# Kernel optimization log

Hardware: AMD Instinct MI355X
Metric: run time of the kernel (lower is better)

## Reference

```python
import math
import jax, jax.numpy as jnp
import numpy as np

B, T, C, H = 2, 2048, 1024, 16
MAX_SEQ = 2048


def _make_pe(max_seq: int, dim: int, base: float = 10000.0) -> np.ndarray:
    pe = np.zeros((max_seq, dim), dtype=np.float32)
    position = np.arange(max_seq, dtype=np.float32)[:, None]
    div_term = np.exp(np.arange(0, dim, 2, dtype=np.float32) * (-math.log(base) / dim))
    pe[:, 0::2] = np.sin(position * div_term)
    pe[:, 1::2] = np.cos(position * div_term)
    return pe


def setup_inputs() -> dict:
    key = jax.random.key(0)
    k1, k2, k3 = jax.random.split(key, 3)
    x = jax.random.normal(k1, (B, T, C), dtype=jnp.float32)
    # torch Linear default init scale ~ 1/sqrt(fan_in)
    w_qkv = jax.random.normal(k2, (3 * C, C), dtype=jnp.float32) / math.sqrt(C)
    w_proj = jax.random.normal(k3, (C, C), dtype=jnp.float32) / math.sqrt(C)
    pe = jnp.asarray(_make_pe(MAX_SEQ, C))
    return {"x": x, "w_qkv": w_qkv, "w_proj": w_proj, "pe": pe}


def reference(x, w_qkv, w_proj, pe):
    b, t, c = x.shape
    h = H
    d = c // h
    # RoPE module adds sinusoidal PE under torch.no_grad() -> stop_gradient
    xp = jax.lax.stop_gradient(x + pe[None, :t, :])
    qkv = xp @ w_qkv.T  # [b, t, 3c]
    q, k, v = jnp.split(qkv, 3, axis=-1)
    q = q.reshape(b, t, h, d).transpose(0, 2, 1, 3)  # bhtd
    k = k.reshape(b, t, h, d).transpose(0, 2, 1, 3)
    v = v.reshape(b, t, h, d).transpose(0, 2, 1, 3)
    att = jnp.einsum("bhqd,bhkd->bhqk", q, k) * (1.0 / math.sqrt(d))
    causal = jnp.tril(jnp.ones((t, t), dtype=bool))  # [t, t]
    att = jnp.where(causal[None, None], att, -jnp.inf)
    att = jax.nn.softmax(att, axis=-1)
    y = jnp.einsum("bhqk,bhkd->bhqd", att, v)
    y = y.transpose(0, 2, 1, 3).reshape(b, t, c)
    return y @ w_proj.T
```

## Files before the change

### kernel.cpp

```cpp
#include <hip/hip_runtime.h>
#include <cstdint>

typedef __bf16 bf16x8 __attribute__((ext_vector_type(8)));
typedef __bf16 bf16x4 __attribute__((ext_vector_type(4)));
typedef float  f32x4  __attribute__((ext_vector_type(4)));

static constexpr int kB = 2, kT = 2048, kC = 1024, kH = 16, kD = 64;
static constexpr int kK = 1024;

__device__ __forceinline__ uint16_t f2bf(float f) {
  uint32_t u = __builtin_bit_cast(uint32_t, f);
  u += 0x7FFFu + ((u >> 16) & 1u);
  return (uint16_t)(u >> 16);
}

__device__ __forceinline__ void gl_lds16(const void* g, void* l) {
  __builtin_amdgcn_global_load_lds((__attribute__((address_space(1))) void*)(void*)g,
                                   (__attribute__((address_space(3))) void*)l, 16, 0, 0);
}

__global__ __launch_bounds__(256) void prep_xpe(const float* __restrict__ x,
                                                const float* __restrict__ pe,
                                                uint16_t* __restrict__ xp) {
  const int i = blockIdx.x * 256 + threadIdx.x;
  const float4 xv = ((const float4*)x)[i];
  const int c4 = i & (kC / 4 - 1);
  const int t = (i / (kC / 4)) & (kT - 1);
  const float4 pv = ((const float4*)pe)[t * (kC / 4) + c4];
  ushort4 o;
  o.x = f2bf(xv.x + pv.x);
  o.y = f2bf(xv.y + pv.y);
  o.z = f2bf(xv.z + pv.z);
  o.w = f2bf(xv.w + pv.w);
  ((ushort4*)xp)[i] = o;
}

__global__ __launch_bounds__(256) void cast_w(const float* __restrict__ w,
                                              uint16_t* __restrict__ o) {
  const int i = blockIdx.x * 256 + threadIdx.x;
  const float4 v = ((const float4*)w)[i];
  ushort4 u;
  u.x = f2bf(v.x); u.y = f2bf(v.y); u.z = f2bf(v.z); u.w = f2bf(v.w);
  ((ushort4*)o)[i] = u;
}

template <int EPI>
__global__ __launch_bounds__(256) void gemm_bt(const uint16_t* __restrict__ A,
                                               const uint16_t* __restrict__ W,
                                               uint16_t* __restrict__ qb,
                                               uint16_t* __restrict__ kb,
                                               uint16_t* __restrict__ vT,
                                               float* __restrict__ out) {
  __shared__ __align__(1024) char lds[EPI == 0 ? 34816 : 32768];
  const int lane = threadIdx.x & 63;
  const int wid = threadIdx.x >> 6;
  const int l15 = lane & 15, l4 = lane >> 4;
  const int wm = wid >> 1, wn = wid & 1;
  const int orig = (int)(blockIdx.y * gridDim.x + blockIdx.x);
  const int xcd = orig & 7, j = orig >> 3;
  const int m0 = (xcd * 4 + (j & 3)) * 128;
  const int n0 = (j >> 2) * 128;

  f32x4 acc[4][4] = {};

  for (int k0 = 0; k0 < kK; k0 += 64) {
#pragma unroll
    for (int jj = 0; jj < 4; ++jj) {
      const int off = wid * 4096 + jj * 1024 + lane * 16;
      const int row = off >> 7;
      const int colb = (off & 127) ^ ((row & 7) << 4);
      gl_lds16((const char*)A + ((size_t)(m0 + row) * kK + k0) * 2 + colb,
               lds + wid * 4096 + jj * 1024);
      gl_lds16((const char*)W + ((size_t)(n0 + row) * kK + k0) * 2 + colb,
               lds + 16384 + wid * 4096 + jj * 1024);
    }
    __syncthreads();
#pragma unroll
    for (int ks = 0; ks < 2; ++ks) {
      bf16x8 af[4], bf_[4];
#pragma unroll
      for (int mt = 0; mt < 4; ++mt) {
        const int r = wm * 64 + mt * 16 + l15;
        const int cb = (l4 * 16 + ks * 64) ^ ((r & 7) << 4);
        af[mt] = *(const bf16x8*)(lds + r * 128 + cb);
      }
#pragma unroll
      for (int nt = 0; nt < 4; ++nt) {
        const int r = wn * 64 + nt * 16 + l15;
        const int cb = (l4 * 16 + ks * 64) ^ ((r & 7) << 4);
        bf_[nt] = *(const bf16x8*)(lds + 16384 + r * 128 + cb);
      }
#pragma unroll
      for (int mt = 0; mt < 4; ++mt)
#pragma unroll
        for (int nt = 0; nt < 4; ++nt)
          acc[mt][nt] = __builtin_amdgcn_mfma_f32_16x16x32_bf16(af[mt], bf_[nt],
                                                                acc[mt][nt], 0, 0, 0);
    }
    __syncthreads();
  }

  if constexpr (EPI == 0) {
    const int sec = n0 >> 10;
    if (sec < 2) {
#pragma unroll
      for (int mt = 0; mt < 4; ++mt)
#pragma unroll
        for (int nt = 0; nt < 4; ++nt)
#pragma unroll
          for (int r = 0; r < 4; ++r) {
            const int m = wm * 64 + mt * 16 + l4 * 4 + r;
            const int n = wn * 64 + nt * 16 + l15;
            *(uint16_t*)(lds + m * 272 + ((n * 2) ^ (((m >> 2) & 3) << 4))) =
                f2bf(acc[mt][nt][r]);
          }
    } else {
#pragma unroll
      for (int mt = 0; mt < 4; ++mt)
#pragma unroll
        for (int nt = 0; nt < 4; ++nt)
#pragma unroll
          for (int r = 0; r < 4; ++r) {
            const int m = wm * 64 + mt * 16 + l4 * 4 + r;
            const int n = wn * 64 + nt * 16 + l15;
            *(uint16_t*)(lds + n * 272 + m * 2) = f2bf(acc[mt][nt][r]);
          }
    }
    __syncthreads();
    const int tid = threadIdx.x;
    const int b = m0 >> 11, tbase = m0 & (kT - 1);
    if (sec < 2) {
      uint16_t* dst = (sec == 0) ? qb : kb;
#pragma unroll
      for (int i = 0; i < 8; ++i) {
        const int g = i * 256 + tid;
        const int ml = g >> 4;
        const int c8 = (g & 15) * 8;
        const bf16x8 v =
            *(const bf16x8*)(lds + ml * 272 + ((c8 * 2) ^ (((ml >> 2) & 3) << 4)));
        const int nn = (n0 & (kC - 1)) + c8;
        const int h = nn >> 6, d = nn & 63;
        *(bf16x8*)(dst + ((size_t)((b * kH + h) * kT + tbase + ml)) * kD + d) = v;
      }
    } else {
#pragma unroll
      for (int i = 0; i < 8; ++i) {
        const int g = i * 256 + tid;
        const int dl = g >> 4;
        const int m8 = (g & 15) * 8;
        const bf16x8 v = *(const bf16x8*)(lds + dl * 272 + m8 * 2);
        const int nn = (n0 & (kC - 1)) + dl;
        const int h = nn >> 6, d = nn & 63;
        *(bf16x8*)(vT + ((size_t)((b * kH + h) * kD + d)) * kT + tbase + m8) = v;
      }
    }
  } else {
#pragma unroll
    for (int mt = 0; mt < 4; ++mt)
#pragma unroll
      for (int nt = 0; nt < 4; ++nt)
#pragma unroll
        for (int r = 0; r < 4; ++r) {
          const int m = m0 + wm * 64 + mt * 16 + l4 * 4 + r;
          const int n = n0 + wn * 64 + nt * 16 + l15;
          out[(size_t)m * kC + n] = acc[mt][nt][r];
        }
  }
}

__global__ __launch_bounds__(256, 4) void attn(const uint16_t* __restrict__ qb,
                                               const uint16_t* __restrict__ kb,
                                               const uint16_t* __restrict__ vT,
                                               uint16_t* __restrict__ y) {
  __shared__ __align__(1024) char lds[40960];
  const int lane = threadIdx.x & 63;
  const int wid = threadIdx.x >> 6;
  const int l15 = lane & 15, l4 = lane >> 4;
  const int bh = blockIdx.x;
  const int qt = (int)(gridDim.y - 1) - (int)blockIdx.y;
  const int q0 = qt * 64 + wid * 16;
  const size_t base = (size_t)bh * kT * kD;
  const uint16_t* Q = qb + base;
  const uint16_t* Kp = kb + base;
  const uint16_t* Vt = vT + base;
  char* P = lds + 32768 + wid * 2048;
  const int xr = (l15 & 7) << 4;

  bf16x8 qf[2];
#pragma unroll
  for (int ks = 0; ks < 2; ++ks) {
    bf16x8 t = *(const bf16x8*)(Q + (size_t)(q0 + l15) * kD + ks * 32 + l4 * 8);
#pragma unroll
    for (int i = 0; i < 8; ++i) t[i] = (__bf16)((float)t[i] * 0.1803368801f);
    qf[ks] = t;
  }

  float m_ = -1e30f, l_ = 0.f;
  f32x4 o[4];
#pragma unroll
  for (int nt = 0; nt < 4; ++nt) o[nt] = (f32x4){0.f, 0.f, 0.f, 0.f};

  const int nkt = qt + 1;

  auto STAGE = [&](int bi, int k0) {
#pragma unroll
    for (int c = 0; c < 2; ++c) {
      const int call = wid * 2 + c;
      const int row = call * 8 + (lane >> 3);
      const int colb = (((lane & 7) ^ ((lane >> 3) & 7)) << 4);
      gl_lds16((const char*)Kp + ((size_t)(k0 + row) * kD) * 2 + colb,
               lds + bi * 8192 + call * 1024);
      gl_lds16((const char*)Vt + ((size_t)row * kT + k0) * 2 + colb,
               lds + 16384 + bi * 8192 + call * 1024);
    }
  };

  int cur = 0;
  STAGE(0, 0);
  for (int kt = 0; kt < nkt; ++kt) {
    const int k0 = kt * 64;
    const bool hasnext = (kt + 1 < nkt);
    if (hasnext) STAGE(cur ^ 1, k0 + 64);
    if (hasnext)
      asm volatile("s_waitcnt vmcnt(4)" ::: "memory");
    else
      asm volatile("s_waitcnt vmcnt(0)" ::: "memory");
    __builtin_amdgcn_s_barrier();
    asm volatile("" ::: "memory");

    const char* Kb = lds + cur * 8192;
    const char* Vb = lds + 16384 + cur * 8192;

    f32x4 s[4] = {};
    __builtin_amdgcn_s_setprio(1);
#pragma unroll
    for (int ks = 0; ks < 2; ++ks)
#pragma unroll
      for (int nt = 0; nt < 4; ++nt) {
        const bf16x8 kf =
            *(const bf16x8*)(Kb + (nt * 16 + l15) * 128 + ((ks * 64 + l4 * 16) ^ xr));
        s[nt] = __builtin_amdgcn_mfma_f32_16x16x32_bf16(kf, qf[ks], s[nt], 0, 0, 0);
      }
    __builtin_amdgcn_s_setprio(0);

    if (kt == nkt - 1) {
      const int qq = q0 + l15;
#pragma unroll
      for (int nt = 0; nt < 4; ++nt)
#pragma unroll
        for (int r = 0; r < 4; ++r)
          if (k0 + nt * 16 + l4 * 4 + r > qq) s[nt][r] = -1e30f;
    }

    float pm = s[0][0];
#pragma unroll
    for (int nt = 0; nt < 4; ++nt)
#pragma unroll
      for (int r = 0; r < 4; ++r) pm = fmaxf(pm, s[nt][r]);
    if (!__all(pm <= m_ + 11.0f)) {
      float rm = fmaxf(pm, __shfl_xor(pm, 16));
      rm = fmaxf(rm, __shfl_xor(rm, 32));
      const float newm = fmaxf(m_, rm);
      const float sc = exp2f(m_ - newm);
      m_ = newm;
      l_ *= sc;
#pragma unroll
      for (int nt = 0; nt < 4; ++nt)
#pragma unroll
        for (int r = 0; r < 4; ++r) o[nt][r] *= sc;
    }
    float ps = 0.f;
#pragma unroll
    for (int nt = 0; nt < 4; ++nt)
#pragma unroll
      for (int r = 0; r < 4; ++r) {
        const float p = exp2f(s[nt][r] - m_);
        s[nt][r] = p;
        ps += p;
      }
    l_ += ps;

#pragma unroll
    for (int nt = 0; nt < 4; ++nt) {
      bf16x4 pk;
#pragma unroll
      for (int r = 0; r < 4; ++r) pk[r] = (__bf16)s[nt][r];
      *(bf16x4*)(P + l15 * 128 + ((nt * 32 + l4 * 8) ^ xr)) = pk;
    }
    asm volatile("s_waitcnt lgkmcnt(0)" ::: "memory");
    __builtin_amdgcn_sched_barrier(0);

    bf16x8 pf[2];
#pragma unroll
    for (int ks = 0; ks < 2; ++ks)
      pf[ks] = *(const bf16x8*)(P + l15 * 128 + ((ks * 64 + l4 * 16) ^ xr));
    __builtin_amdgcn_s_setprio(1);
#pragma unroll
    for (int ks = 0; ks < 2; ++ks)
#pragma unroll
      for (int nt = 0; nt < 4; ++nt) {
        const bf16x8 vf =
            *(const bf16x8*)(Vb + (nt * 16 + l15) * 128 + ((ks * 64 + l4 * 16) ^ xr));
        o[nt] = __builtin_amdgcn_mfma_f32_16x16x32_bf16(vf, pf[ks], o[nt], 0, 0, 0);
      }
    __builtin_amdgcn_s_setprio(0);

    __builtin_amdgcn_s_barrier();
    asm volatile("" ::: "memory");
    cur ^= 1;
  }

  l_ += __shfl_xor(l_, 16);
  l_ += __shfl_xor(l_, 32);
  const float inv = 1.0f / l_;
  const int b = bh >> 4, h = bh & 15;
  const int q = q0 + l15;
#pragma unroll
  for (int nt = 0; nt < 4; ++nt) {
    bf16x4 yv;
#pragma unroll
    for (int r = 0; r < 4; ++r) yv[r] = (__bf16)(o[nt][r] * inv);
    *(bf16x4*)(y + ((size_t)(b * kT + q)) * kC + h * kD + nt * 16 + l4 * 4) = yv;
  }
}

extern "C" void kernel_launch(void* const* d_in, const int* in_sizes, int n_in,
                              void* d_out, int out_size, void* d_ws, size_t ws_size,
                              hipStream_t stream) {
  const float* x = (const float*)d_in[0];
  const float* wqkv = (const float*)d_in[1];
  const float* wproj = (const float*)d_in[2];
  const float* pe = (const float*)d_in[3];

  char* ws = (char*)d_ws;
  uint16_t* xp = (uint16_t*)(ws);
  uint16_t* wq = (uint16_t*)(ws + (size_t)(8u << 20));
  uint16_t* wp = (uint16_t*)(ws + (size_t)(14u << 20));
  uint16_t* qbuf = (uint16_t*)(ws + (size_t)(16u << 20));
  uint16_t* kbuf = (uint16_t*)(ws + (size_t)(24u << 20));
  uint16_t* vTb = (uint16_t*)(ws + (size_t)(32u << 20));

  prep_xpe<<<dim3(kB * kT * kC / 4 / 256), 256, 0, stream>>>(x, pe, xp);
  cast_w<<<dim3(3 * kC * kC / 4 / 256), 256, 0, stream>>>(wqkv, wq);
  cast_w<<<dim3(kC * kC / 4 / 256), 256, 0, stream>>>(wproj, wp);

  gemm_bt<0><<<dim3(32, 24), 256, 0, stream>>>(xp, wq, qbuf, kbuf, vTb, nullptr);

  attn<<<dim3(kB * kH, kT / 64), 256, 0, stream>>>(qbuf, kbuf, vTb, xp);

  gemm_bt<1><<<dim3(32, 8), 256, 0, stream>>>(xp, wp, nullptr, nullptr, nullptr,
                                              (float*)d_out);
}
```

Before: 119.9 us.

## Replace QKV GEMM with 256x256-tile, 8-wave, double-buffered pipelined kernel

The QKV projection moves to a new kernel with 256x256 output tiles, 512 threads and 128KB of LDS. Global-to-LDS loads are double-buffered and interleaved with MFMA work in eight quadrant phases, using explicit vmcnt waits, barriers and s_setprio. This is meant to hide load latency and raise MFMA utilisation compared with the old single-buffered 128x128 kernel. Q and K epilogues now write straight to global with scalar stores, while V still transposes through LDS. The result is only 192 workgroups, and the uncoalesced Q/K stores and heavy LDS use may cost occupancy and bandwidth.

```diff
diff --git a/kernel.cpp b/kernel.cpp
--- a/kernel.cpp
+++ b/kernel.cpp
@@ -44,14 +44,158 @@
   ((ushort4*)o)[i] = u;
 }
 
-template <int EPI>
-__global__ __launch_bounds__(256) void gemm_bt(const uint16_t* __restrict__ A,
-                                               const uint16_t* __restrict__ W,
-                                               uint16_t* __restrict__ qb,
-                                               uint16_t* __restrict__ kb,
-                                               uint16_t* __restrict__ vT,
-                                               float* __restrict__ out) {
-  __shared__ __align__(1024) char lds[EPI == 0 ? 34816 : 32768];
+__global__ __launch_bounds__(512, 2) void gemm_qkv(const uint16_t* __restrict__ A,
+                                                   const uint16_t* __restrict__ W,
+                                                   uint16_t* __restrict__ qb,
+                                                   uint16_t* __restrict__ kb,
+                                                   uint16_t* __restrict__ vT) {
+  __shared__ __align__(1024) char lds[131072];
+  const int tid = threadIdx.x;
+  const int lane = tid & 63;
+  const int wid = tid >> 6;
+  const int l15 = lane & 15, l4 = lane >> 4;
+  const int WM = wid >> 2, WN = wid & 3;
+  const int orig = (int)blockIdx.x;
+  const int xcd = orig & 7, j = orig >> 3;
+  const int m0 = (xcd * 2 + (j & 1)) * 256;
+  const int n0 = (j >> 1) * 256;
+  constexpr int NKT = kK / 64;
+  constexpr int NIT = NKT / 2;
+
+  f32x4 acc[4][4][2] = {};
+
+  auto stage = [&](int isA, int buf, int half, int kt) {
+#pragma unroll
+    for (int c = 0; c < 2; ++c) {
+      const int off = (c * 512 + tid) * 16;
+      const int lr = off >> 7, cbl = off & 127;
+      const size_t grow = (size_t)((isA ? m0 : n0) + half * 128 + lr) * kK + kt * 64;
+      gl_lds16((const char*)(isA ? A : W) + grow * 2 + (cbl ^ ((lr & 7) << 4)),
+               lds + (isA ? 0 : 65536) + buf * 32768 + half * 16384 + off);
+    }
+  };
+  auto bar = [&] {
+    asm volatile("" ::: "memory");
+    __builtin_amdgcn_s_barrier();
+    asm volatile("" ::: "memory");
+  };
+
+  stage(1, 0, 0, 0); stage(0, 0, 0, 0);
+  stage(1, 0, 1, 0); stage(0, 0, 1, 0);
+  stage(1, 1, 0, 1); stage(0, 1, 0, 1);
+
+  for (int i = 0; i < NIT; ++i) {
+#pragma unroll
+    for (int p = 0; p < 8; ++p) {
+      constexpr int ISA[8] = {1, 0, 1, 0, 1, 0, 1, 0};
+      constexpr int HLF[8] = {1, 1, 0, 0, 1, 1, 0, 0};
+      constexpr int TOF[8] = {1, 1, 2, 2, 2, 2, 3, 3};
+      const int qr = (p >> 1) & 1, qc = p & 1;
+      const int cbuf = (p >> 2) & 1, q4 = p & 3;
+      {
+        int kt = 2 * i + TOF[p];
+        if (kt > NKT - 1) kt = NKT - 1;
+        stage(ISA[p], TOF[p] & 1, HLF[p], kt);
+      }
+      const char* Ab = lds + cbuf * 32768 + qr * 16384;
+      const char* Bb = lds + 65536 + cbuf * 32768 + qc * 16384;
+      bf16x8 af[2][4], bfr[2][2];
+      auto reads = [&] {
+#pragma unroll
+        for (int ks = 0; ks < 2; ++ks) {
+#pragma unroll
+          for (int mt = 0; mt < 4; ++mt) {
+            const int lr = WM * 64 + mt * 16 + l15;
+            af[ks][mt] = *(const bf16x8*)(Ab + lr * 128 +
+                                          ((ks * 64 + l4 * 16) ^ ((lr & 7) << 4)));
+          }
+#pragma unroll
+          for (int nt = 0; nt < 2; ++nt) {
+            const int lr = WN * 32 + nt * 16 + l15;
+            bfr[ks][nt] = *(const bf16x8*)(Bb + lr * 128 +
+                                           ((ks * 64 + l4 * 16) ^ ((lr & 7) << 4)));
+          }
+        }
+      };
+      if (p == 0 || p == 4) {
+        asm volatile("s_waitcnt vmcnt(6)" ::: "memory");
+        bar();
+        reads();
+      } else {
+        reads();
+        bar();
+      }
+      __builtin_amdgcn_s_setprio(1);
+#pragma unroll
+      for (int ks = 0; ks < 2; ++ks)
+#pragma unroll
+        for (int mt = 0; mt < 4; ++mt)
+#pragma unroll
+          for (int nt = 0; nt < 2; ++nt)
+            acc[q4][mt][nt] = __builtin_amdgcn_mfma_f32_16x16x32_bf16(
+                af[ks][mt], bfr[ks][nt], acc[q4][mt][nt], 0, 0, 0);
+      __builtin_amdgcn_s_setprio(0);
+      bar();
+    }
+  }
+  asm volatile("s_waitcnt vmcnt(0)" ::: "memory");
+  bar();
+
+  const int sec = n0 >> 10;
+  const int b = m0 >> 11, tb = m0 & (kT - 1);
+  if (sec < 2) {
+    uint16_t* dst = (sec == 0) ? qb : kb;
+#pragma unroll
+    for (int q4 = 0; q4 < 4; ++q4) {
+      const int qr = q4 >> 1, qc = q4 & 1;
+#pragma unroll
+      for (int mt = 0; mt < 4; ++mt)
+#pragma unroll
+        for (int nt = 0; nt < 2; ++nt)
+#pragma unroll
+          for (int r = 0; r < 4; ++r) {
+            const int m = qr * 128 + WM * 64 + mt * 16 + l4 * 4 + r;
+            const int nn = (n0 & (kC - 1)) + qc * 128 + WN * 32 + nt * 16 + l15;
+            const int h = nn >> 6, d = nn & 63;
+            dst[((size_t)((b * kH + h) * kT + tb + m)) * kD + d] =
+                f2bf(acc[q4][mt][nt][r]);
+          }
+    }
+  } else {
+#pragma unroll
+    for (int q4 = 0; q4 < 4; ++q4) {
+      const int qr = q4 >> 1, qc = q4 & 1;
+#pragma unroll
+      for (int mt = 0; mt < 4; ++mt)
+#pragma unroll
+        for (int nt = 0; nt < 2; ++nt) {
+          const int nl = qc * 128 + WN * 32 + nt * 16 + l15;
+          const int mb2 = (qr * 128 + WM * 64 + mt * 16 + l4 * 4) * 2;
+          ushort4 pk;
+          pk.x = f2bf(acc[q4][mt][nt][0]);
+          pk.y = f2bf(acc[q4][mt][nt][1]);
+          pk.z = f2bf(acc[q4][mt][nt][2]);
+          pk.w = f2bf(acc[q4][mt][nt][3]);
+          *(ushort4*)(lds + nl * 512 + (mb2 ^ ((nl & 7) << 4))) = pk;
+        }
+    }
+    bar();
+#pragma unroll
+    for (int it = 0; it < 16; ++it) {
+      const int chunk = it * 512 + tid;
+      const int nr = chunk >> 5, mb = (chunk & 31) * 16;
+      const bf16x8 v = *(const bf16x8*)(lds + nr * 512 + (mb ^ ((nr & 7) << 4)));
+      const int nn = (n0 - 2048) + nr;
+      const int h = nn >> 6, d = nn & 63;
+      *(bf16x8*)(vT + ((size_t)((b * kH + h) * kD + d)) * kT + tb + (chunk & 31) * 8) = v;
+    }
+  }
+}
+
+__global__ __launch_bounds__(256) void gemm_proj(const uint16_t* __restrict__ A,
+                                                 const uint16_t* __restrict__ W,
+                                                 float* __restrict__ out) {
+  __shared__ __align__(1024) char lds[32768];
   const int lane = threadIdx.x & 63;
   const int wid = threadIdx.x >> 6;
   const int l15 = lane & 15, l4 = lane >> 4;
@@ -100,72 +244,16 @@
     __syncthreads();
   }
 
-  if constexpr (EPI == 0) {
-    const int sec = n0 >> 10;
-    if (sec < 2) {
-#pragma unroll
-      for (int mt = 0; mt < 4; ++mt)
-#pragma unroll
-        for (int nt = 0; nt < 4; ++nt)
-#pragma unroll
-          for (int r = 0; r < 4; ++r) {
-            const int m = wm * 64 + mt * 16 + l4 * 4 + r;
-            const int n = wn * 64 + nt * 16 + l15;
-            *(uint16_t*)(lds + m * 272 + ((n * 2) ^ (((m >> 2) & 3) << 4))) =
-                f2bf(acc[mt][nt][r]);
-          }
-    } else {
-#pragma unroll
-      for (int mt = 0; mt < 4; ++mt)
-#pragma unroll
-        for (int nt = 0; nt < 4; ++nt)
-#pragma unroll
-          for (int r = 0; r < 4; ++r) {
-            const int m = wm * 64 + mt * 16 + l4 * 4 + r;
-            const int n = wn * 64 + nt * 16 + l15;
-            *(uint16_t*)(lds + n * 272 + m * 2) = f2bf(acc[mt][nt][r]);
-          }
-    }
-    __syncthreads();
-    const int tid = threadIdx.x;
-    const int b = m0 >> 11, tbase = m0 & (kT - 1);
-    if (sec < 2) {
-      uint16_t* dst = (sec == 0) ? qb : kb;
-#pragma unroll
-      for (int i = 0; i < 8; ++i) {
-        const int g = i * 256 + tid;
-        const int ml = g >> 4;
-        const int c8 = (g & 15) * 8;
-        const bf16x8 v =
-            *(const bf16x8*)(lds + ml * 272 + ((c8 * 2) ^ (((ml >> 2) & 3) << 4)));
-        const int nn = (n0 & (kC - 1)) + c8;
-        const int h = nn >> 6, d = nn & 63;
-        *(bf16x8*)(dst + ((size_t)((b * kH + h) * kT + tbase + ml)) * kD + d) = v;
-      }
-    } else {
-#pragma unroll
-      for (int i = 0; i < 8; ++i) {
-        const int g = i * 256 + tid;
-        const int dl = g >> 4;
-        const int m8 = (g & 15) * 8;
-        const bf16x8 v = *(const bf16x8*)(lds + dl * 272 + m8 * 2);
-        const int nn = (n0 & (kC - 1)) + dl;
-        const int h = nn >> 6, d = nn & 63;
-        *(bf16x8*)(vT + ((size_t)((b * kH + h) * kD + d)) * kT + tbase + m8) = v;
-      }
-    }
-  } else {
-#pragma unroll
-    for (int mt = 0; mt < 4; ++mt)
-#pragma unroll
-      for (int nt = 0; nt < 4; ++nt)
-#pragma unroll
-        for (int r = 0; r < 4; ++r) {
-          const int m = m0 + wm * 64 + mt * 16 + l4 * 4 + r;
-          const int n = n0 + wn * 64 + nt * 16 + l15;
-          out[(size_t)m * kC + n] = acc[mt][nt][r];
-        }
-  }
+#pragma unroll
+  for (int mt = 0; mt < 4; ++mt)
+#pragma unroll
+    for (int nt = 0; nt < 4; ++nt)
+#pragma unroll
+      for (int r = 0; r < 4; ++r) {
+        const int m = m0 + wm * 64 + mt * 16 + l4 * 4 + r;
+        const int n = n0 + wn * 64 + nt * 16 + l15;
+        out[(size_t)m * kC + n] = acc[mt][nt][r];
+      }
 }
 
 __global__ __launch_bounds__(256, 4) void attn(const uint16_t* __restrict__ qb,
@@ -344,10 +432,9 @@
   cast_w<<<dim3(3 * kC * kC / 4 / 256), 256, 0, stream>>>(wqkv, wq);
   cast_w<<<dim3(kC * kC / 4 / 256), 256, 0, stream>>>(wproj, wp);
 
-  gemm_bt<0><<<dim3(32, 24), 256, 0, stream>>>(xp, wq, qbuf, kbuf, vTb, nullptr);
+  gemm_qkv<<<dim3(192), 512, 0, stream>>>(xp, wq, qbuf, kbuf, vTb);
 
   attn<<<dim3(kB * kH, kT / 64), 256, 0, stream>>>(qbuf, kbuf, vTb, xp);
 
-  gemm_bt<1><<<dim3(32, 8), 256, 0, stream>>>(xp, wp, nullptr, nullptr, nullptr,
-                                              (float*)d_out);
-}
+  gemm_proj<<<dim3(32, 8), 256, 0, stream>>>(xp, wp, (float*)d_out);
+}
```

Result: faster. 113.6 us (-5.2%).

## Merge prep casts into one kernel and rewrite QKV GEMM with 256x256 double-buffered tiles

Applied to the files above, without the earlier changes.

The three preprocessing kernels (x+pe cast, two weight casts) are fused into one launch to cut launch overhead. The QKV projection becomes a dedicated 512-thread kernel with 256x256 tiles, double-buffered LDS (128KB) staged asynchronously via global_load_lds with explicit vmcnt waits and setprio around the MFMA bursts, so loads overlap compute. The epilogue writes q/k straight from registers with scalar stores and transposes V through LDS. It trades the earlier coalesced q/k epilogue and occupancy for more reuse and a grid of only 192 blocks.

```diff
diff --git a/kernel.cpp b/kernel.cpp
--- a/kernel.cpp
+++ b/kernel.cpp
@@ -19,39 +19,179 @@
                                    (__attribute__((address_space(3))) void*)l, 16, 0, 0);
 }
 
-__global__ __launch_bounds__(256) void prep_xpe(const float* __restrict__ x,
+__global__ __launch_bounds__(256) void prep_all(const float* __restrict__ x,
                                                 const float* __restrict__ pe,
-                                                uint16_t* __restrict__ xp) {
+                                                const float* __restrict__ wqkv,
+                                                const float* __restrict__ wproj,
+                                                uint16_t* __restrict__ xp,
+                                                uint16_t* __restrict__ wq,
+                                                uint16_t* __restrict__ wp) {
+  constexpr int NX = kB * kT * kC / 4;
+  constexpr int NWQ = 3 * kC * kC / 4;
   const int i = blockIdx.x * 256 + threadIdx.x;
-  const float4 xv = ((const float4*)x)[i];
-  const int c4 = i & (kC / 4 - 1);
-  const int t = (i / (kC / 4)) & (kT - 1);
-  const float4 pv = ((const float4*)pe)[t * (kC / 4) + c4];
-  ushort4 o;
-  o.x = f2bf(xv.x + pv.x);
-  o.y = f2bf(xv.y + pv.y);
-  o.z = f2bf(xv.z + pv.z);
-  o.w = f2bf(xv.w + pv.w);
-  ((ushort4*)xp)[i] = o;
-}
-
-__global__ __launch_bounds__(256) void cast_w(const float* __restrict__ w,
-                                              uint16_t* __restrict__ o) {
-  const int i = blockIdx.x * 256 + threadIdx.x;
-  const float4 v = ((const float4*)w)[i];
-  ushort4 u;
-  u.x = f2bf(v.x); u.y = f2bf(v.y); u.z = f2bf(v.z); u.w = f2bf(v.w);
-  ((ushort4*)o)[i] = u;
-}
-
-template <int EPI>
-__global__ __launch_bounds__(256) void gemm_bt(const uint16_t* __restrict__ A,
-                                               const uint16_t* __restrict__ W,
-                                               uint16_t* __restrict__ qb,
-                                               uint16_t* __restrict__ kb,
-                                               uint16_t* __restrict__ vT,
-                                               float* __restrict__ out) {
-  __shared__ __align__(1024) char lds[EPI == 0 ? 34816 : 32768];
+  if (i < NX) {
+    const float4 xv = ((const float4*)x)[i];
+    const int c4 = i & (kC / 4 - 1);
+    const int t = (i / (kC / 4)) & (kT - 1);
+    const float4 pv = ((const float4*)pe)[t * (kC / 4) + c4];
+    ushort4 o;
+    o.x = f2bf(xv.x + pv.x);
+    o.y = f2bf(xv.y + pv.y);
+    o.z = f2bf(xv.z + pv.z);
+    o.w = f2bf(xv.w + pv.w);
+    ((ushort4*)xp)[i] = o;
+  } else if (i < NX + NWQ) {
+    const int j = i - NX;
+    const float4 v = ((const float4*)wqkv)[j];
+    ushort4 u;
+    u.x = f2bf(v.x); u.y = f2bf(v.y); u.z = f2bf(v.z); u.w = f2bf(v.w);
+    ((ushort4*)wq)[j] = u;
+  } else {
+    const int j = i - NX - NWQ;
+    const float4 v = ((const float4*)wproj)[j];
+    ushort4 u;
+    u.x = f2bf(v.x); u.y = f2bf(v.y); u.z = f2bf(v.z); u.w = f2bf(v.w);
+    ((ushort4*)wp)[j] = u;
+  }
+}
+
+__global__ __launch_bounds__(512, 2) void gemm_qkv(const uint16_t* __restrict__ A,
+                                                   const uint16_t* __restrict__ W,
+                                                   uint16_t* __restrict__ qb,
+                                                   uint16_t* __restrict__ kb,
+                                                   uint16_t* __restrict__ vT) {
+  __shared__ __align__(1024) char lds[131072];
+  const int tid = threadIdx.x;
+  const int lane = tid & 63;
+  const int wid = tid >> 6;
+  const int l15 = lane & 15, l4 = lane >> 4;
+  const int WM = wid >> 2, WN = wid & 3;
+  const int orig = (int)blockIdx.x;
+  const int xcd = orig & 7, j = orig >> 3;
+  const int m0 = (xcd * 2 + (j & 1)) * 256;
+  const int n0 = (j >> 1) * 256;
+
+  f32x4 acc[2][4][4] = {};
+  bf16x8 bfp[2][4];
+
+  auto stage = [&](int isA, int buf, int kt) {
+#pragma unroll
+    for (int c = 0; c < 4; ++c) {
+      const int off = (c * 512 + tid) * 16;
+      const int lr = off >> 7, cbl = off & 127;
+      const size_t grow = (size_t)((isA ? m0 : n0) + lr) * kK + kt * 64;
+      gl_lds16((const char*)(isA ? A : W) + grow * 2 + (cbl ^ ((lr & 7) << 4)),
+               lds + (isA ? 0 : 65536) + buf * 32768 + off);
+    }
+  };
+
+#define QKV_PHASE(CBUF, H, SA, SBUF, KT, VM)                                      \
+  {                                                                               \
+    stage(SA, SBUF, KT);                                                          \
+    if (VM == 4)                                                                  \
+      asm volatile("s_waitcnt vmcnt(4)" ::: "memory");                            \
+    else                                                                          \
+      asm volatile("s_waitcnt vmcnt(8)" ::: "memory");                            \
+    __builtin_amdgcn_s_barrier();                                                 \
+    asm volatile("" ::: "memory");                                                \
+    const char* Ab = lds + (CBUF)*32768;                                          \
+    const char* Bb = lds + 65536 + (CBUF)*32768;                                  \
+    if ((H) == 0) {                                                               \
+      _Pragma("unroll") for (int ks = 0; ks < 2; ++ks)                            \
+          _Pragma("unroll") for (int nt = 0; nt < 4; ++nt) {                      \
+        const int lr = WN * 64 + nt * 16 + l15;                                   \
+        bfp[ks][nt] = *(const bf16x8*)(Bb + lr * 128 +                            \
+                                       ((ks * 64 + l4 * 16) ^ ((lr & 7) << 4)));  \
+      }                                                                           \
+    }                                                                             \
+    _Pragma("unroll") for (int ks = 0; ks < 2; ++ks) {                            \
+      bf16x8 af[4];                                                               \
+      _Pragma("unroll") for (int mt = 0; mt < 4; ++mt) {                          \
+        const int lr = (H)*128 + WM * 64 + mt * 16 + l15;                         \
+        af[mt] = *(const bf16x8*)(Ab + lr * 128 +                                 \
+                                  ((ks * 64 + l4 * 16) ^ ((lr & 7) << 4)));       \
+      }                                                                           \
+      __builtin_amdgcn_s_setprio(1);                                              \
+      _Pragma("unroll") for (int mt = 0; mt < 4; ++mt)                            \
+          _Pragma("unroll") for (int nt = 0; nt < 4; ++nt)                        \
+              acc[H][mt][nt] = __builtin_amdgcn_mfma_f32_16x16x32_bf16(           \
+                  af[mt], bfp[ks][nt], acc[H][mt][nt], 0, 0, 0);                  \
+      __builtin_amdgcn_s_setprio(0);                                              \
+    }                                                                             \
+    asm volatile("" ::: "memory");                                                \
+    __builtin_amdgcn_s_barrier();                                                 \
+    asm volatile("" ::: "memory");                                                \
+  }
+
+  stage(1, 0, 0);
+  stage(0, 0, 0);
+
+  for (int i = 0; i < 8; ++i) {
+    const int ktb1 = 2 * i + 1;
+    const int ktb0 = (2 * i + 2 > 15) ? 15 : 2 * i + 2;
+    QKV_PHASE(0, 0, 1, 1, ktb1, 4);
+    QKV_PHASE(0, 1, 0, 1, ktb1, 8);
+    QKV_PHASE(1, 0, 1, 0, ktb0, 4);
+    QKV_PHASE(1, 1, 0, 0, ktb0, 8);
+  }
+  asm volatile("s_waitcnt vmcnt(0)" ::: "memory");
+  __builtin_amdgcn_s_barrier();
+  asm volatile("" ::: "memory");
+
+  const int sec = n0 >> 10;
+  const int b = m0 >> 11, tb = m0 & (kT - 1);
+  if (sec < 2) {
+    uint16_t* dst = (sec == 0) ? qb : kb;
+#pragma unroll
+    for (int h = 0; h < 2; ++h)
+#pragma unroll
+      for (int mt = 0; mt < 4; ++mt)
+#pragma unroll
+        for (int nt = 0; nt < 4; ++nt)
+#pragma unroll
+          for (int r = 0; r < 4; ++r) {
+            const int m = h * 128 + WM * 64 + mt * 16 + l4 * 4 + r;
+            const int nn = (n0 & (kC - 1)) + WN * 64 + nt * 16 + l15;
+            const int hh = nn >> 6, d = nn & 63;
+            dst[((size_t)((b * kH + hh) * kT + tb + m)) * kD + d] =
+                f2bf(acc[h][mt][nt][r]);
+          }
+  } else {
+#pragma unroll
+    for (int h = 0; h < 2; ++h)
+#pragma unroll
+      for (int mt = 0; mt < 4; ++mt)
+#pragma unroll
+        for (int nt = 0; nt < 4; ++nt) {
+          const int nl = WN * 64 + nt * 16 + l15;
+          const int mb2 = (h * 128 + WM * 64 + mt * 16 + l4 * 4) * 2;
+          ushort4 pk;
+          pk.x = f2bf(acc[h][mt][nt][0]);
+          pk.y = f2bf(acc[h][mt][nt][1]);
+          pk.z = f2bf(acc[h][mt][nt][2]);
+          pk.w = f2bf(acc[h][mt][nt][3]);
+          *(ushort4*)(lds + nl * 512 + (mb2 ^ ((nl & 7) << 4))) = pk;
+        }
+    asm volatile("" ::: "memory");
+    __builtin_amdgcn_s_barrier();
+    asm volatile("" ::: "memory");
+#pragma unroll
+    for (int it = 0; it < 16; ++it) {
+      const int chunk = it * 512 + tid;
+      const int nr = chunk >> 5, mb = (chunk & 31) * 16;
+      const bf16x8 v = *(const bf16x8*)(lds + nr * 512 + (mb ^ ((nr & 7) << 4)));
+      const int nn = (n0 - 2048) + nr;
+      const int hh = nn >> 6, d = nn & 63;
+      *(bf16x8*)(vT + ((size_t)((b * kH + hh) * kD + d)) * kT + tb + (chunk & 31) * 8) = v;
+    }
+  }
+#undef QKV_PHASE
+}
+
+__global__ __launch_bounds__(256) void gemm_proj(const uint16_t* __restrict__ A,
+                                                 const uint16_t* __restrict__ W,
+                                                 float* __restrict__ out) {
+  __shared__ __align__(1024) char lds[32768];
   const int lane = threadIdx.x & 63;
   const int wid = threadIdx.x >> 6;
   const int l15 = lane & 15, l4 = lane >> 4;
@@ -100,72 +240,16 @@
     __syncthreads();
   }
 
-  if constexpr (EPI == 0) {
-    const int sec = n0 >> 10;
-    if (sec < 2) {
-#pragma unroll
-      for (int mt = 0; mt < 4; ++mt)
-#pragma unroll
-        for (int nt = 0; nt < 4; ++nt)
-#pragma unroll
-          for (int r = 0; r < 4; ++r) {
-            const int m = wm * 64 + mt * 16 + l4 * 4 + r;
-            const int n = wn * 64 + nt * 16 + l15;
-            *(uint16_t*)(lds + m * 272 + ((n * 2) ^ (((m >> 2) & 3) << 4))) =
-                f2bf(acc[mt][nt][r]);
-          }
-    } else {
-#pragma unroll
-      for (int mt = 0; mt < 4; ++mt)
-#pragma unroll
-        for (int nt = 0; nt < 4; ++nt)
-#pragma unroll
-          for (int r = 0; r < 4; ++r) {
-            const int m = wm * 64 + mt * 16 + l4 * 4 + r;
-            const int n = wn * 64 + nt * 16 + l15;
-            *(uint16_t*)(lds + n * 272 + m * 2) = f2bf(acc[mt][nt][r]);
-          }
-    }
-    __syncthreads();
-    const int tid = threadIdx.x;
-    const int b = m0 >> 11, tbase = m0 & (kT - 1);
-    if (sec < 2) {
-      uint16_t* dst = (sec == 0) ? qb : kb;
-#pragma unroll
-      for (int i = 0; i < 8; ++i) {
-        const int g = i * 256 + tid;
-        const int ml = g >> 4;
-        const int c8 = (g & 15) * 8;
-        const bf16x8 v =
-            *(const bf16x8*)(lds + ml * 272 + ((c8 * 2) ^ (((ml >> 2) & 3) << 4)));
-        const int nn = (n0 & (kC - 1)) + c8;
-        const int h = nn >> 6, d = nn & 63;
-        *(bf16x8*)(dst + ((size_t)((b * kH + h) * kT + tbase + ml)) * kD + d) = v;
-      }
-    } else {
-#pragma unroll
-      for (int i = 0; i < 8; ++i) {
-        const int g = i * 256 + tid;
-        const int dl = g >> 4;
-        const int m8 = (g & 15) * 8;
-        const bf16x8 v = *(const bf16x8*)(lds + dl * 272 + m8 * 2);
-        const int nn = (n0 & (kC - 1)) + dl;
-        const int h = nn >> 6, d = nn & 63;
-        *(bf16x8*)(vT + ((size_t)((b * kH + h) * kD + d)) * kT + tbase + m8) = v;
-      }
-    }
-  } else {
-#pragma unroll
-    for (int mt = 0; mt < 4; ++mt)
-#pragma unroll
-      for (int nt = 0; nt < 4; ++nt)
-#pragma unroll
-        for (int r = 0; r < 4; ++r) {
-          const int m = m0 + wm * 64 + mt * 16 + l4 * 4 + r;
-          const int n = n0 + wn * 64 + nt * 16 + l15;
-          out[(size_t)m * kC + n] = acc[mt][nt][r];
-        }
-  }
+#pragma unroll
+  for (int mt = 0; mt < 4; ++mt)
+#pragma unroll
+    for (int nt = 0; nt < 4; ++nt)
+#pragma unroll
+      for (int r = 0; r < 4; ++r) {
+        const int m = m0 + wm * 64 + mt * 16 + l4 * 4 + r;
+        const int n = n0 + wn * 64 + nt * 16 + l15;
+        out[(size_t)m * kC + n] = acc[mt][nt][r];
+      }
 }
 
 __global__ __launch_bounds__(256, 4) void attn(const uint16_t* __restrict__ qb,
@@ -340,14 +424,11 @@
   uint16_t* kbuf = (uint16_t*)(ws + (size_t)(24u << 20));
   uint16_t* vTb = (uint16_t*)(ws + (size_t)(32u << 20));
 
-  prep_xpe<<<dim3(kB * kT * kC / 4 / 256), 256, 0, stream>>>(x, pe, xp);
-  cast_w<<<dim3(3 * kC * kC / 4 / 256), 256, 0, stream>>>(wqkv, wq);
-  cast_w<<<dim3(kC * kC / 4 / 256), 256, 0, stream>>>(wproj, wp);
-
-  gemm_bt<0><<<dim3(32, 24), 256, 0, stream>>>(xp, wq, qbuf, kbuf, vTb, nullptr);
+  prep_all<<<dim3(8192), 256, 0, stream>>>(x, pe, wqkv, wproj, xp, wq, wp);
+
+  gemm_qkv<<<dim3(192), 512, 0, stream>>>(xp, wq, qbuf, kbuf, vTb);
 
   attn<<<dim3(kB * kH, kT / 64), 256, 0, stream>>>(qbuf, kbuf, vTb, xp);
 
-  gemm_bt<1><<<dim3(32, 8), 256, 0, stream>>>(xp, wp, nullptr, nullptr, nullptr,
-                                              (float*)d_out);
-}
+  gemm_proj<<<dim3(32, 8), 256, 0, stream>>>(xp, wp, (float*)d_out);
+}
```

Measured after the change: 107.7 us. 10.2% less time.
